# Kernel optimization log

Measured on AMD Instinct MI355X. Metric: run time of the kernel, lower is better.

Reference implementation:

```python
import jax, jax.numpy as jnp
import numpy as np

N_NODES = 100000
N_EDGES = 1250000
D_FEAT = 64


def setup_inputs() -> dict:
    key = jax.random.key(0)
    kx, ke = jax.random.split(key)
    x = jax.random.normal(kx, (N_NODES, D_FEAT), dtype=jnp.float32)
    edge_index = jax.random.randint(ke, (2, N_EDGES), 0, N_NODES, dtype=jnp.int64)
    return {"x": x, "edge_index": edge_index}


def reference(x, edge_index):
    # propagate: scatter_nested gathers x[idxj] grouped by destination idxi
    # (a ragged per-node neighbor set); the module's sum_nested reduces each
    # group. Expressed densely and jit-ably as gather + segment-sum.
    idxi = edge_index[0, :]  # destination nodes
    idxj = edge_index[1, :]  # source nodes
    messages = x[idxj]  # [E, D] edge-level gather (memory-bound)
    out = jax.ops.segment_sum(messages, idxi, num_segments=N_NODES)  # [N, D]
    return out
```

## Files before the change

### kernel.cpp

```cpp
#include <hip/hip_runtime.h>
#include <hip/hip_fp16.h>

#define N_NODES 100000
#define N_EDGES 1250000
#define D_FEAT  64

#define NPB     392
#define NBINS   256
#define BCAP    6144
#define HALF    196
#define HCAP    3328
#define K23B    (NBINS * 2)
#define EPB     5120
#define EPT     10
#define K1B     ((N_EDGES + EPB - 1) / EPB)
#define OVF_CAP 32768
#define XH_INTS (N_NODES * (D_FEAT / 2))

__global__ __launch_bounds__(256) void kconv_kernel(
        const float* __restrict__ x, unsigned int* __restrict__ xh,
        int* __restrict__ gcursor) {
    int t = blockIdx.x * 256 + threadIdx.x;
    if (t < 256 + 16) gcursor[t] = 0;
    const float2* x2 = (const float2*)x;
    int total = XH_INTS;
    int stride = gridDim.x * 256;
    for (int i = t; i < total; i += stride) {
        float2 v = x2[i];
        __half2 h = __floats2half2_rn(v.x, v.y);
        xh[i] = *(unsigned int*)&h;
    }
}

__global__ __launch_bounds__(512) void k1_bin_kernel(
        const int* __restrict__ idxi, const int* __restrict__ idxj,
        int* __restrict__ gcursor, int* __restrict__ ovfcnt,
        int* __restrict__ ovf, int* __restrict__ binbuf) {
    __shared__ int hist[NBINS];
    __shared__ int runstart[NBINS];
    __shared__ int gbase[NBINS];
    __shared__ int cur[NBINS];
    __shared__ int staged[EPB];
    __shared__ unsigned char sbin[EPB];
    int t = threadIdx.x;
    if (t < NBINS) hist[t] = 0;
    __syncthreads();

    int base = blockIdx.x * EPB;
    int n = N_EDGES - base; if (n > EPB) n = EPB;

    int d[EPT], s[EPT], bn[EPT];
#pragma unroll
    for (int j = 0; j < EPT; ++j) {
        int i = t + j * 512;
        if (i < n) { d[j] = idxi[base + i]; s[j] = idxj[base + i]; }
        else       { d[j] = -1; s[j] = 0; }
    }
#pragma unroll
    for (int j = 0; j < EPT; ++j) {
        bn[j] = (d[j] >= 0) ? (d[j] / NPB) : -1;
        if (bn[j] >= 0) atomicAdd(&hist[bn[j]], 1);
    }
    __syncthreads();

    if (t < 64) {
        int b0 = t * 4;
        int h0 = hist[b0], h1 = hist[b0 + 1], h2 = hist[b0 + 2], h3 = hist[b0 + 3];
        int s01 = h0 + h1;
        int sum = s01 + h2 + h3;
        int inc = sum;
#pragma unroll
        for (int off = 1; off < 64; off <<= 1) {
            int u = __shfl_up(inc, off, 64);
            if (t >= off) inc += u;
        }
        int ex = inc - sum;
        runstart[b0]     = ex;
        runstart[b0 + 1] = ex + h0;
        runstart[b0 + 2] = ex + s01;
        runstart[b0 + 3] = ex + s01 + h2;
    }
    __syncthreads();

    if (t < NBINS) {
        int h = hist[t];
        gbase[t] = h ? atomicAdd(&gcursor[t], h) : 0;
        cur[t] = 0;
    }
    __syncthreads();

#pragma unroll
    for (int j = 0; j < EPT; ++j) {
        if (bn[j] >= 0) {
            int idx = runstart[bn[j]] + atomicAdd(&cur[bn[j]], 1);
            staged[idx] = ((d[j] - bn[j] * NPB) << 17) | s[j];
            sbin[idx] = (unsigned char)bn[j];
        }
    }
    __syncthreads();

    for (int i = t; i < n; i += 512) {
        int b = sbin[i];
        int p = staged[i];
        int tgt = gbase[b] + (i - runstart[b]);
        if (tgt < BCAP) {
            binbuf[b * BCAP + tgt] = p;
        } else {
            int op = atomicAdd(ovfcnt, 1);
            if (op < OVF_CAP) { ovf[2 * op] = b * NPB + (p >> 17); ovf[2 * op + 1] = p & 0x1FFFF; }
        }
    }
}

__device__ __forceinline__ float4 cvt4(uint2 u) {
    __half2 a = *reinterpret_cast<__half2*>(&u.x);
    __half2 b = *reinterpret_cast<__half2*>(&u.y);
    float2 fa = __half22float2(a);
    float2 fb = __half22float2(b);
    return make_float4(fa.x, fa.y, fb.x, fb.y);
}

__global__ __launch_bounds__(1024, 8) void k23_fp16_kernel(
        const float* __restrict__ x, const unsigned int* __restrict__ xh,
        const int* __restrict__ gcursor, const int* __restrict__ binbuf,
        const int* __restrict__ ovfcnt, const int* __restrict__ ovf,
        float* __restrict__ out) {
    __shared__ int cnt[HALF];
    __shared__ int excl[HALF];
    __shared__ int cur[HALF];
    __shared__ int srt[HCAP];
    int blk = blockIdx.x;
    int bin = blk >> 1;
    int hi  = blk & 1;
    int lobase = hi * HALF;
    int t = threadIdx.x;
    if (t < HALF) cnt[t] = 0;
    __syncthreads();

    int n = gcursor[bin];
    if (n > BCAP) n = BCAP;
    const int* src = binbuf + (size_t)bin * BCAP;

    int p[6];
#pragma unroll
    for (int j = 0; j < 6; ++j) {
        int i = t + j * 1024;
        p[j] = (i < n) ? src[i] : -1;
    }
#pragma unroll
    for (int j = 0; j < 6; ++j) {
        if (p[j] >= 0) {
            int loc = (p[j] >> 17) - lobase;
            if ((unsigned)loc < HALF) atomicAdd(&cnt[loc], 1);
            else p[j] = -1;
        }
    }
    __syncthreads();

    if (t < 64) {
        int h[4];
        int sum = 0;
#pragma unroll
        for (int q = 0; q < 4; ++q) {
            int b = t * 4 + q;
            h[q] = (b < HALF) ? cnt[b] : 0;
            sum += h[q];
        }
        int inc = sum;
#pragma unroll
        for (int off = 1; off < 64; off <<= 1) {
            int u = __shfl_up(inc, off, 64);
            if (t >= off) inc += u;
        }
        int ex = inc - sum;
#pragma unroll
        for (int q = 0; q < 4; ++q) {
            int b = t * 4 + q;
            if (b < HALF) { excl[b] = ex; cur[b] = 0; }
            ex += h[q];
        }
    }
    __syncthreads();

#pragma unroll
    for (int j = 0; j < 6; ++j) {
        if (p[j] >= 0) {
            int loc = (p[j] >> 17) - lobase;
            int pos = excl[loc] + atomicAdd(&cur[loc], 1);
            if (pos < HCAP) srt[pos] = p[j] & 0x1FFFF;
        }
    }
    __syncthreads();

    int sg = t >> 4, c4 = t & 15;
    const uint2* xp = (const uint2*)xh;
#pragma unroll
    for (int i2 = 0; i2 < 4; ++i2) {
        int dl = sg + (i2 << 6);
        if (dl >= HALF) break;
        int node = bin * NPB + lobase + dl;
        int k = excl[dl];
        int end = k + cnt[dl];
        if (end > HCAP) end = HCAP;
        float4 acc = make_float4(0.f, 0.f, 0.f, 0.f);
        for (; k + 8 <= end; k += 8) {
            uint2 u0 = xp[(size_t)srt[k]     * 16 + c4];
            uint2 u1 = xp[(size_t)srt[k + 1] * 16 + c4];
            uint2 u2 = xp[(size_t)srt[k + 2] * 16 + c4];
            uint2 u3 = xp[(size_t)srt[k + 3] * 16 + c4];
            uint2 u4 = xp[(size_t)srt[k + 4] * 16 + c4];
            uint2 u5 = xp[(size_t)srt[k + 5] * 16 + c4];
            uint2 u6 = xp[(size_t)srt[k + 6] * 16 + c4];
            uint2 u7 = xp[(size_t)srt[k + 7] * 16 + c4];
            float4 v0 = cvt4(u0), v1 = cvt4(u1), v2 = cvt4(u2), v3 = cvt4(u3);
            float4 v4 = cvt4(u4), v5 = cvt4(u5), v6 = cvt4(u6), v7 = cvt4(u7);
            acc.x += ((v0.x + v1.x) + (v2.x + v3.x)) + ((v4.x + v5.x) + (v6.x + v7.x));
            acc.y += ((v0.y + v1.y) + (v2.y + v3.y)) + ((v4.y + v5.y) + (v6.y + v7.y));
            acc.z += ((v0.z + v1.z) + (v2.z + v3.z)) + ((v4.z + v5.z) + (v6.z + v7.z));
            acc.w += ((v0.w + v1.w) + (v2.w + v3.w)) + ((v4.w + v5.w) + (v6.w + v7.w));
        }
        if (k + 4 <= end) {
            uint2 u0 = xp[(size_t)srt[k]     * 16 + c4];
            uint2 u1 = xp[(size_t)srt[k + 1] * 16 + c4];
            uint2 u2 = xp[(size_t)srt[k + 2] * 16 + c4];
            uint2 u3 = xp[(size_t)srt[k + 3] * 16 + c4];
            float4 v0 = cvt4(u0), v1 = cvt4(u1), v2 = cvt4(u2), v3 = cvt4(u3);
            acc.x += (v0.x + v1.x) + (v2.x + v3.x);
            acc.y += (v0.y + v1.y) + (v2.y + v3.y);
            acc.z += (v0.z + v1.z) + (v2.z + v3.z);
            acc.w += (v0.w + v1.w) + (v2.w + v3.w);
            k += 4;
        }
        for (; k < end; ++k) {
            float4 v0 = cvt4(xp[(size_t)srt[k] * 16 + c4]);
            acc.x += v0.x; acc.y += v0.y; acc.z += v0.z; acc.w += v0.w;
        }
        if (node < N_NODES)
            ((float4*)out)[(size_t)node * 16 + c4] = acc;
    }

    __syncthreads();
    int novf = *ovfcnt;
    if (novf > 0) {
        __threadfence();
        if (novf > OVF_CAP) novf = OVF_CAP;
        int lo = bin * NPB + lobase;
        for (int e = t; e < novf; e += 1024) {
            int dnode = ovf[2 * e];
            if ((unsigned)(dnode - lo) < HALF && dnode < N_NODES) {
                int snode = ovf[2 * e + 1];
                const float* vsrc = x + (size_t)snode * D_FEAT;
                float* o = out + (size_t)dnode * D_FEAT;
                for (int f = 0; f < D_FEAT; ++f) atomicAdd(o + f, vsrc[f]);
            }
        }
    }
}

__global__ __launch_bounds__(1024, 8) void k23_fused_kernel(
        const float* __restrict__ x, const int* __restrict__ gcursor,
        const int* __restrict__ binbuf, const int* __restrict__ ovfcnt,
        const int* __restrict__ ovf, float* __restrict__ out) {
    __shared__ int cnt[HALF];
    __shared__ int excl[HALF];
    __shared__ int cur[HALF];
    __shared__ int srt[HCAP];
    int blk = blockIdx.x;
    int bin = blk >> 1;
    int hi  = blk & 1;
    int lobase = hi * HALF;
    int t = threadIdx.x;
    if (t < HALF) cnt[t] = 0;
    __syncthreads();

    int n = gcursor[bin];
    if (n > BCAP) n = BCAP;
    const int* src = binbuf + (size_t)bin * BCAP;

    int p[6];
#pragma unroll
    for (int j = 0; j < 6; ++j) {
        int i = t + j * 1024;
        p[j] = (i < n) ? src[i] : -1;
    }
#pragma unroll
    for (int j = 0; j < 6; ++j) {
        if (p[j] >= 0) {
            int loc = (p[j] >> 17) - lobase;
            if ((unsigned)loc < HALF) atomicAdd(&cnt[loc], 1);
            else p[j] = -1;
        }
    }
    __syncthreads();

    if (t < 64) {
        int h[4];
        int sum = 0;
#pragma unroll
        for (int q = 0; q < 4; ++q) {
            int b = t * 4 + q;
            h[q] = (b < HALF) ? cnt[b] : 0;
            sum += h[q];
        }
        int inc = sum;
#pragma unroll
        for (int off = 1; off < 64; off <<= 1) {
            int u = __shfl_up(inc, off, 64);
            if (t >= off) inc += u;
        }
        int ex = inc - sum;
#pragma unroll
        for (int q = 0; q < 4; ++q) {
            int b = t * 4 + q;
            if (b < HALF) { excl[b] = ex; cur[b] = 0; }
            ex += h[q];
        }
    }
    __syncthreads();

#pragma unroll
    for (int j = 0; j < 6; ++j) {
        if (p[j] >= 0) {
            int loc = (p[j] >> 17) - lobase;
            int pos = excl[loc] + atomicAdd(&cur[loc], 1);
            if (pos < HCAP) srt[pos] = p[j] & 0x1FFFF;
        }
    }
    __syncthreads();

    int sg = t >> 4, c4 = t & 15;
    const float4* xp = (const float4*)x;
#pragma unroll
    for (int i2 = 0; i2 < 4; ++i2) {
        int dl = sg + (i2 << 6);
        if (dl >= HALF) break;
        int node = bin * NPB + lobase + dl;
        int k = excl[dl];
        int end = k + cnt[dl];
        if (end > HCAP) end = HCAP;
        float4 acc = make_float4(0.f, 0.f, 0.f, 0.f);
        for (; k + 8 <= end; k += 8) {
            int a0 = srt[k],     a1 = srt[k + 1], a2 = srt[k + 2], a3 = srt[k + 3];
            int a4 = srt[k + 4], a5 = srt[k + 5], a6 = srt[k + 6], a7 = srt[k + 7];
            float4 v0 = xp[a0 * 16 + c4];
            float4 v1 = xp[a1 * 16 + c4];
            float4 v2 = xp[a2 * 16 + c4];
            float4 v3 = xp[a3 * 16 + c4];
            float4 v4 = xp[a4 * 16 + c4];
            float4 v5 = xp[a5 * 16 + c4];
            float4 v6 = xp[a6 * 16 + c4];
            float4 v7 = xp[a7 * 16 + c4];
            acc.x += ((v0.x + v1.x) + (v2.x + v3.x)) + ((v4.x + v5.x) + (v6.x + v7.x));
            acc.y += ((v0.y + v1.y) + (v2.y + v3.y)) + ((v4.y + v5.y) + (v6.y + v7.y));
            acc.z += ((v0.z + v1.z) + (v2.z + v3.z)) + ((v4.z + v5.z) + (v6.z + v7.z));
            acc.w += ((v0.w + v1.w) + (v2.w + v3.w)) + ((v4.w + v5.w) + (v6.w + v7.w));
        }
        if (k + 4 <= end) {
            int a0 = srt[k], a1 = srt[k + 1], a2 = srt[k + 2], a3 = srt[k + 3];
            float4 v0 = xp[a0 * 16 + c4];
            float4 v1 = xp[a1 * 16 + c4];
            float4 v2 = xp[a2 * 16 + c4];
            float4 v3 = xp[a3 * 16 + c4];
            acc.x += (v0.x + v1.x) + (v2.x + v3.x);
            acc.y += (v0.y + v1.y) + (v2.y + v3.y);
            acc.z += (v0.z + v1.z) + (v2.z + v3.z);
            acc.w += (v0.w + v1.w) + (v2.w + v3.w);
            k += 4;
        }
        for (; k < end; ++k) {
            float4 v0 = xp[srt[k] * 16 + c4];
            acc.x += v0.x; acc.y += v0.y; acc.z += v0.z; acc.w += v0.w;
        }
        if (node < N_NODES)
            ((float4*)out)[(size_t)node * 16 + c4] = acc;
    }

    __syncthreads();
    int novf = *ovfcnt;
    if (novf > 0) {
        __threadfence();
        if (novf > OVF_CAP) novf = OVF_CAP;
        int lo = bin * NPB + lobase;
        for (int e = t; e < novf; e += 1024) {
            int dnode = ovf[2 * e];
            if ((unsigned)(dnode - lo) < HALF && dnode < N_NODES) {
                int snode = ovf[2 * e + 1];
                const float* vsrc = x + (size_t)snode * D_FEAT;
                float* o = out + (size_t)dnode * D_FEAT;
                for (int f = 0; f < D_FEAT; ++f) atomicAdd(o + f, vsrc[f]);
            }
        }
    }
}


__global__ __launch_bounds__(256) void zero_f4_kernel(float* __restrict__ out, int n4) {
    int i = blockIdx.x * blockDim.x + threadIdx.x;
    if (i < n4) ((float4*)out)[i] = make_float4(0.f, 0.f, 0.f, 0.f);
}

__global__ __launch_bounds__(256) void scatter_add_kernel(const float* __restrict__ x,
                                                          const int* __restrict__ idxi,
                                                          const int* __restrict__ idxj,
                                                          float* __restrict__ out) {
    int t = blockIdx.x * blockDim.x + threadIdx.x;
    int e = t >> 4;
    if (e >= N_EDGES) return;
    int fo = (t & 15) << 2;
    int dst = idxi[e];
    int src = idxj[e];
    const float4 v = *(const float4*)(x + (size_t)src * D_FEAT + fo);
    float* o = out + (size_t)dst * D_FEAT + fo;
    atomicAdd(o + 0, v.x);
    atomicAdd(o + 1, v.y);
    atomicAdd(o + 2, v.z);
    atomicAdd(o + 3, v.w);
}

extern "C" void kernel_launch(void* const* d_in, const int* in_sizes, int n_in,
                              void* d_out, int out_size, void* d_ws, size_t ws_size,
                              hipStream_t stream) {
    const float* x  = (const float*)d_in[0];
    const int*   ei = (const int*)d_in[1];
    const int*   idxi = ei;
    const int*   idxj = ei + N_EDGES;
    float* out = (float*)d_out;

    {
        size_t need = (256 + 16 + 2 * (size_t)OVF_CAP + (size_t)XH_INTS +
                       (size_t)NBINS * BCAP) * sizeof(int);
        if (ws_size >= need) {
            int* gcursor = (int*)d_ws;
            int* ovfcnt  = gcursor + 256;
            int* ovf     = ovfcnt + 16;
            unsigned int* xh = (unsigned int*)(ovf + 2 * OVF_CAP);
            int* binbuf  = (int*)(xh + XH_INTS);

            kconv_kernel<<<2048, 256, 0, stream>>>(x, xh, gcursor);
            k1_bin_kernel<<<K1B, 512, 0, stream>>>(idxi, idxj, gcursor, ovfcnt, ovf, binbuf);
            k23_fp16_kernel<<<K23B, 1024, 0, stream>>>(x, xh, gcursor, binbuf, ovfcnt, ovf, out);
            return;
        }
    }

    {
        size_t need = (256 + 16 + 2 * (size_t)OVF_CAP +
                       (size_t)NBINS * BCAP) * sizeof(int);
        if (ws_size >= need) {
            int* gcursor = (int*)d_ws;
            int* ovfcnt  = gcursor + 256;
            int* ovf     = ovfcnt + 16;
            int* binbuf  = ovf + 2 * OVF_CAP;

            hipMemsetAsync(gcursor, 0, (256 + 16) * sizeof(int), stream);
            k1_bin_kernel<<<K1B, 512, 0, stream>>>(idxi, idxj, gcursor, ovfcnt, ovf, binbuf);
            k23_fused_kernel<<<K23B, 1024, 0, stream>>>(x, gcursor, binbuf, ovfcnt, ovf, out);
            return;
        }
    }

    int n4 = (N_NODES * D_FEAT) / 4;
    zero_f4_kernel<<<(n4 + 255) / 256, 256, 0, stream>>>(out, n4);
    long long total_threads = (long long)N_EDGES * 16;
    scatter_add_kernel<<<(int)((total_threads + 255) / 256), 256, 0, stream>>>(x, idxi, idxj, out);
}
```

Before: 130.5 us.

## Merge fp16 conversion into binning kernel and widen gather loads to 16 bytes

The standalone x-to-fp16 conversion kernel is removed, and its work now runs on extra blocks appended to the binning kernel, so both run concurrently within one launch. A memset replaces the cursor zeroing the conversion kernel used to do. The fp16 gather now has 8 threads per node, each loading a 16-byte uint4 holding 8 halves, in place of 16 threads loading 8 bytes each, and the unroll depth drops from 8 to 4 in both gather kernels. This cuts one kernel launch and the serialisation between conversion and binning, and halves the gather load instruction count, at the cost of fewer loads in flight per thread.

```diff
diff --git a/kernel.cpp b/kernel.cpp
--- a/kernel.cpp
+++ b/kernel.cpp
@@ -14,34 +14,34 @@
 #define EPB     5120
 #define EPT     10
 #define K1B     ((N_EDGES + EPB - 1) / EPB)
+#define CONVB   256
 #define OVF_CAP 32768
 #define XH_INTS (N_NODES * (D_FEAT / 2))
 
-__global__ __launch_bounds__(256) void kconv_kernel(
-        const float* __restrict__ x, unsigned int* __restrict__ xh,
-        int* __restrict__ gcursor) {
-    int t = blockIdx.x * 256 + threadIdx.x;
-    if (t < 256 + 16) gcursor[t] = 0;
-    const float2* x2 = (const float2*)x;
-    int total = XH_INTS;
-    int stride = gridDim.x * 256;
-    for (int i = t; i < total; i += stride) {
-        float2 v = x2[i];
-        __half2 h = __floats2half2_rn(v.x, v.y);
-        xh[i] = *(unsigned int*)&h;
-    }
-}
-
-__global__ __launch_bounds__(512) void k1_bin_kernel(
+__global__ __launch_bounds__(512) void k1_bin_conv_kernel(
         const int* __restrict__ idxi, const int* __restrict__ idxj,
         int* __restrict__ gcursor, int* __restrict__ ovfcnt,
-        int* __restrict__ ovf, int* __restrict__ binbuf) {
+        int* __restrict__ ovf, int* __restrict__ binbuf,
+        const float* __restrict__ x, unsigned int* __restrict__ xh) {
     __shared__ int hist[NBINS];
     __shared__ int runstart[NBINS];
     __shared__ int gbase[NBINS];
     __shared__ int cur[NBINS];
     __shared__ int staged[EPB];
     __shared__ unsigned char sbin[EPB];
+
+    if (blockIdx.x >= K1B) {
+        int t0 = (blockIdx.x - K1B) * 512 + threadIdx.x;
+        int stride = CONVB * 512;
+        const float2* x2 = (const float2*)x;
+        for (int i = t0; i < XH_INTS; i += stride) {
+            float2 v = x2[i];
+            __half2 h = __floats2half2_rn(v.x, v.y);
+            xh[i] = *(unsigned int*)&h;
+        }
+        return;
+    }
+
     int t = threadIdx.x;
     if (t < NBINS) hist[t] = 0;
     __syncthreads();
@@ -112,12 +112,15 @@
     }
 }
 
-__device__ __forceinline__ float4 cvt4(uint2 u) {
-    __half2 a = *reinterpret_cast<__half2*>(&u.x);
-    __half2 b = *reinterpret_cast<__half2*>(&u.y);
-    float2 fa = __half22float2(a);
-    float2 fb = __half22float2(b);
-    return make_float4(fa.x, fa.y, fb.x, fb.y);
+__device__ __forceinline__ void cvt8(uint4 u, float4& a, float4& b) {
+    __half2 h0 = *reinterpret_cast<__half2*>(&u.x);
+    __half2 h1 = *reinterpret_cast<__half2*>(&u.y);
+    __half2 h2 = *reinterpret_cast<__half2*>(&u.z);
+    __half2 h3 = *reinterpret_cast<__half2*>(&u.w);
+    float2 f0 = __half22float2(h0), f1 = __half22float2(h1);
+    float2 f2 = __half22float2(h2), f3 = __half22float2(h3);
+    a = make_float4(f0.x, f0.y, f1.x, f1.y);
+    b = make_float4(f2.x, f2.y, f3.x, f3.y);
 }
 
 __global__ __launch_bounds__(1024, 8) void k23_fp16_kernel(
@@ -192,51 +195,42 @@
     }
     __syncthreads();
 
-    int sg = t >> 4, c4 = t & 15;
-    const uint2* xp = (const uint2*)xh;
-#pragma unroll
-    for (int i2 = 0; i2 < 4; ++i2) {
-        int dl = sg + (i2 << 6);
-        if (dl >= HALF) break;
+    int sg = t >> 3, c8 = t & 7;
+    const uint4* xp = (const uint4*)xh;
+    for (int dl = sg; dl < HALF; dl += 128) {
         int node = bin * NPB + lobase + dl;
         int k = excl[dl];
         int end = k + cnt[dl];
         if (end > HCAP) end = HCAP;
-        float4 acc = make_float4(0.f, 0.f, 0.f, 0.f);
-        for (; k + 8 <= end; k += 8) {
-            uint2 u0 = xp[(size_t)srt[k]     * 16 + c4];
-            uint2 u1 = xp[(size_t)srt[k + 1] * 16 + c4];
-            uint2 u2 = xp[(size_t)srt[k + 2] * 16 + c4];
-            uint2 u3 = xp[(size_t)srt[k + 3] * 16 + c4];
-            uint2 u4 = xp[(size_t)srt[k + 4] * 16 + c4];
-            uint2 u5 = xp[(size_t)srt[k + 5] * 16 + c4];
-            uint2 u6 = xp[(size_t)srt[k + 6] * 16 + c4];
-            uint2 u7 = xp[(size_t)srt[k + 7] * 16 + c4];
-            float4 v0 = cvt4(u0), v1 = cvt4(u1), v2 = cvt4(u2), v3 = cvt4(u3);
-            float4 v4 = cvt4(u4), v5 = cvt4(u5), v6 = cvt4(u6), v7 = cvt4(u7);
-            acc.x += ((v0.x + v1.x) + (v2.x + v3.x)) + ((v4.x + v5.x) + (v6.x + v7.x));
-            acc.y += ((v0.y + v1.y) + (v2.y + v3.y)) + ((v4.y + v5.y) + (v6.y + v7.y));
-            acc.z += ((v0.z + v1.z) + (v2.z + v3.z)) + ((v4.z + v5.z) + (v6.z + v7.z));
-            acc.w += ((v0.w + v1.w) + (v2.w + v3.w)) + ((v4.w + v5.w) + (v6.w + v7.w));
-        }
-        if (k + 4 <= end) {
-            uint2 u0 = xp[(size_t)srt[k]     * 16 + c4];
-            uint2 u1 = xp[(size_t)srt[k + 1] * 16 + c4];
-            uint2 u2 = xp[(size_t)srt[k + 2] * 16 + c4];
-            uint2 u3 = xp[(size_t)srt[k + 3] * 16 + c4];
-            float4 v0 = cvt4(u0), v1 = cvt4(u1), v2 = cvt4(u2), v3 = cvt4(u3);
-            acc.x += (v0.x + v1.x) + (v2.x + v3.x);
-            acc.y += (v0.y + v1.y) + (v2.y + v3.y);
-            acc.z += (v0.z + v1.z) + (v2.z + v3.z);
-            acc.w += (v0.w + v1.w) + (v2.w + v3.w);
-            k += 4;
+        float4 accA = make_float4(0.f, 0.f, 0.f, 0.f);
+        float4 accB = make_float4(0.f, 0.f, 0.f, 0.f);
+        for (; k + 4 <= end; k += 4) {
+            uint4 u0 = xp[(size_t)srt[k]     * 8 + c8];
+            uint4 u1 = xp[(size_t)srt[k + 1] * 8 + c8];
+            uint4 u2 = xp[(size_t)srt[k + 2] * 8 + c8];
+            uint4 u3 = xp[(size_t)srt[k + 3] * 8 + c8];
+            float4 a0, b0, a1, b1, a2, b2, a3, b3;
+            cvt8(u0, a0, b0); cvt8(u1, a1, b1); cvt8(u2, a2, b2); cvt8(u3, a3, b3);
+            accA.x += (a0.x + a1.x) + (a2.x + a3.x);
+            accA.y += (a0.y + a1.y) + (a2.y + a3.y);
+            accA.z += (a0.z + a1.z) + (a2.z + a3.z);
+            accA.w += (a0.w + a1.w) + (a2.w + a3.w);
+            accB.x += (b0.x + b1.x) + (b2.x + b3.x);
+            accB.y += (b0.y + b1.y) + (b2.y + b3.y);
+            accB.z += (b0.z + b1.z) + (b2.z + b3.z);
+            accB.w += (b0.w + b1.w) + (b2.w + b3.w);
         }
         for (; k < end; ++k) {
-            float4 v0 = cvt4(xp[(size_t)srt[k] * 16 + c4]);
-            acc.x += v0.x; acc.y += v0.y; acc.z += v0.z; acc.w += v0.w;
-        }
-        if (node < N_NODES)
-            ((float4*)out)[(size_t)node * 16 + c4] = acc;
+            uint4 u0 = xp[(size_t)srt[k] * 8 + c8];
+            float4 a0, b0;
+            cvt8(u0, a0, b0);
+            accA.x += a0.x; accA.y += a0.y; accA.z += a0.z; accA.w += a0.w;
+            accB.x += b0.x; accB.y += b0.y; accB.z += b0.z; accB.w += b0.w;
+        }
+        if (node < N_NODES) {
+            ((float4*)out)[(size_t)node * 16 + (c8 << 1)]     = accA;
+            ((float4*)out)[(size_t)node * 16 + (c8 << 1) + 1] = accB;
+        }
     }
 
     __syncthreads();
@@ -339,23 +333,7 @@
         int end = k + cnt[dl];
         if (end > HCAP) end = HCAP;
         float4 acc = make_float4(0.f, 0.f, 0.f, 0.f);
-        for (; k + 8 <= end; k += 8) {
-            int a0 = srt[k],     a1 = srt[k + 1], a2 = srt[k + 2], a3 = srt[k + 3];
-            int a4 = srt[k + 4], a5 = srt[k + 5], a6 = srt[k + 6], a7 = srt[k + 7];
-            float4 v0 = xp[a0 * 16 + c4];
-            float4 v1 = xp[a1 * 16 + c4];
-            float4 v2 = xp[a2 * 16 + c4];
-            float4 v3 = xp[a3 * 16 + c4];
-            float4 v4 = xp[a4 * 16 + c4];
-            float4 v5 = xp[a5 * 16 + c4];
-            float4 v6 = xp[a6 * 16 + c4];
-            float4 v7 = xp[a7 * 16 + c4];
-            acc.x += ((v0.x + v1.x) + (v2.x + v3.x)) + ((v4.x + v5.x) + (v6.x + v7.x));
-            acc.y += ((v0.y + v1.y) + (v2.y + v3.y)) + ((v4.y + v5.y) + (v6.y + v7.y));
-            acc.z += ((v0.z + v1.z) + (v2.z + v3.z)) + ((v4.z + v5.z) + (v6.z + v7.z));
-            acc.w += ((v0.w + v1.w) + (v2.w + v3.w)) + ((v4.w + v5.w) + (v6.w + v7.w));
-        }
-        if (k + 4 <= end) {
+        for (; k + 4 <= end; k += 4) {
             int a0 = srt[k], a1 = srt[k + 1], a2 = srt[k + 2], a3 = srt[k + 3];
             float4 v0 = xp[a0 * 16 + c4];
             float4 v1 = xp[a1 * 16 + c4];
@@ -365,7 +343,6 @@
             acc.y += (v0.y + v1.y) + (v2.y + v3.y);
             acc.z += (v0.z + v1.z) + (v2.z + v3.z);
             acc.w += (v0.w + v1.w) + (v2.w + v3.w);
-            k += 4;
         }
         for (; k < end; ++k) {
             float4 v0 = xp[srt[k] * 16 + c4];
@@ -436,9 +413,11 @@
             unsigned int* xh = (unsigned int*)(ovf + 2 * OVF_CAP);
             int* binbuf  = (int*)(xh + XH_INTS);
 
-            kconv_kernel<<<2048, 256, 0, stream>>>(x, xh, gcursor);
-            k1_bin_kernel<<<K1B, 512, 0, stream>>>(idxi, idxj, gcursor, ovfcnt, ovf, binbuf);
-            k23_fp16_kernel<<<K23B, 1024, 0, stream>>>(x, xh, gcursor, binbuf, ovfcnt, ovf, out);
+            hipMemsetAsync(gcursor, 0, (256 + 16) * sizeof(int), stream);
+            k1_bin_conv_kernel<<<K1B + CONVB, 512, 0, stream>>>(
+                idxi, idxj, gcursor, ovfcnt, ovf, binbuf, x, xh);
+            k23_fp16_kernel<<<K23B, 1024, 0, stream>>>(x, xh, gcursor, binbuf,
+                                                       ovfcnt, ovf, out);
             return;
         }
     }
@@ -453,8 +432,10 @@
             int* binbuf  = ovf + 2 * OVF_CAP;
 
             hipMemsetAsync(gcursor, 0, (256 + 16) * sizeof(int), stream);
-            k1_bin_kernel<<<K1B, 512, 0, stream>>>(idxi, idxj, gcursor, ovfcnt, ovf, binbuf);
-            k23_fused_kernel<<<K23B, 1024, 0, stream>>>(x, gcursor, binbuf, ovfcnt, ovf, out);
+            k1_bin_conv_kernel<<<K1B, 512, 0, stream>>>(
+                idxi, idxj, gcursor, ovfcnt, ovf, binbuf, x, (unsigned int*)0);
+            k23_fused_kernel<<<K23B, 1024, 0, stream>>>(x, gcursor, binbuf,
+                                                        ovfcnt, ovf, out);
             return;
         }
     }
```

Measured after the change: 130.5 us. No clear change (-0.0%).
